# Kernel optimization log

Measured on AMD Instinct MI355X. Metric: run time of the kernel, lower is better.

## Reference

```python
import jax, jax.numpy as jnp
import numpy as np

BN_EPS = 1e-5
LRELU_SLOPE = 0.01  # torch nn.LeakyReLU default


def setup_inputs() -> dict:
    key = jax.random.key(0)
    k1, k2 = jax.random.split(key)
    B, N, Cin, Cout = 8, 4096, 64, 128
    x = jax.random.normal(k1, (B, N, Cin), dtype=jnp.float32)
    W = jax.random.normal(k2, (Cout, Cin), dtype=jnp.float32) * (1.0 / np.sqrt(Cin))
    gamma = jnp.ones((Cout,), dtype=jnp.float32)
    beta = jnp.zeros((Cout,), dtype=jnp.float32)
    return {"x": x, "W": W, "gamma": gamma, "beta": beta, "k": 8}


def _knn_gather_max(x, k):
    # x: [B, N, C]. Negative squared euclidean distance (larger = closer).
    xx = jnp.sum(x * x, axis=-1)                       # [B, N]
    inner = jnp.einsum('bnc,bmc->bnm', x, x)           # [B, N, N]
    neg_dist = 2.0 * inner - xx[:, :, None] - xx[:, None, :]
    idx = jax.lax.top_k(neg_dist, k)[1]                # [B, N, k] int32
    # gather neighbor features: neigh[b,n,j,c] = x[b, idx[b,n,j], c]
    neigh = jax.vmap(lambda xb, ib: xb[ib])(x, idx)    # [B, N, k, C]
    return jnp.max(neigh, axis=2)                      # [B, N, C]


def reference(x, W, gamma, beta, k):
    feat = _knn_gather_max(x, k)                       # [B, N, Cin]
    y = jnp.einsum('bnc,oc->bno', feat, W)             # 1x1 Conv1d, no bias -> [B, N, Cout]
    # BatchNorm1d in training mode: stats over batch and spatial (N) dims
    mean = jnp.mean(y, axis=(0, 1))
    var = jnp.var(y, axis=(0, 1))
    y = (y - mean) * jax.lax.rsqrt(var + BN_EPS) * gamma + beta
    return jnp.where(y >= 0, y, LRELU_SLOPE * y)       # LeakyReLU
```

## Files before the change

kernel.cpp:

```cpp
#include <hip/hip_runtime.h>
#include <hip/hip_bf16.h>

#define NPTS 4096
#define CIN 64
#define COUT 128
#define BATCH 8
#define KNN 8
#define NCH 12
#define NCT 24
#define TOTROWS (BATCH * NPTS)

using short8 = __attribute__((ext_vector_type(8))) short;
using f32x4  = __attribute__((ext_vector_type(4))) float;

__device__ __forceinline__ unsigned short f2bf_rne(float f) {
    unsigned int u = __float_as_uint(f);
    unsigned int r = (u + 0x7fffu + ((u >> 16) & 1u)) >> 16;
    return (unsigned short)r;
}

__device__ __forceinline__ unsigned int umed3(unsigned int a, unsigned int b, unsigned int c) {
    unsigned int d;
    asm("v_med3_u32 %0, %1, %2, %3" : "=v"(d) : "v"(a), "v"(b), "v"(c));
    return d;
}

__global__ __launch_bounds__(256) void prep_kernel(const float* __restrict__ x,
                                                   unsigned short* __restrict__ xpack,
                                                   float* __restrict__ xxn,
                                                   double* __restrict__ xxd) {
    int i   = blockIdx.x * 256 + threadIdx.x;
    int row = i >> 3, g = i & 7;
    const float* src = x + (size_t)row * CIN + g * 8;
    float4 v0 = *(const float4*)src;
    float4 v1 = *(const float4*)(src + 4);
    float f[8] = {v0.x, v0.y, v0.z, v0.w, v1.x, v1.y, v1.z, v1.w};

    unsigned int h[8];
    double s = 0.0;
    #pragma unroll
    for (int j = 0; j < 8; ++j) {
        h[j] = (unsigned int)f2bf_rne(f[j]);
        s += (double)f[j] * (double)f[j];
    }
    uint4 hi;
    hi.x = h[0] | (h[1] << 16); hi.y = h[2] | (h[3] << 16);
    hi.z = h[4] | (h[5] << 16); hi.w = h[6] | (h[7] << 16);
    *(uint4*)&xpack[(size_t)row * 64 + g * 8] = hi;

    s += __shfl_xor(s, 1);
    s += __shfl_xor(s, 2);
    s += __shfl_xor(s, 4);
    if (g == 0) { xxn[row] = 1000.f - (float)s; xxd[row] = s; }
}

__global__ __launch_bounds__(256, 6) void knn_cand_kernel(const unsigned short* __restrict__ xpack,
                                                          const float* __restrict__ xxn,
                                                          int* __restrict__ cand) {
    __shared__ __align__(16) unsigned int mK[4096];
    __shared__ float xxs[128];
    unsigned short* BUF0 = (unsigned short*)mK;
    unsigned short* BUF1 = BUF0 + 4096;

    const int tid  = threadIdx.x;
    const int n0   = blockIdx.x * 64;
    const int half = blockIdx.y;
    const int b    = blockIdx.z;
    const int wave = tid >> 6;
    const int lane = tid & 63;
    const int lrow = lane & 15;
    const int quad = lane >> 4;
    const int colbase = half << 11;

    const unsigned short* xp = xpack + ((size_t)b << 12) * 64;
    const float* xnn = xxn + (b << 12);

    const int arow = n0 + wave * 16 + lrow;
    short8 ah0 = *(const short8*)&xp[arow * 64 + quad * 8];
    short8 ah1 = *(const short8*)&xp[arow * 64 + 32 + quad * 8];

    unsigned int keys[4][8];
    #pragma unroll
    for (int r = 0; r < 4; ++r)
        #pragma unroll
        for (int j = 0; j < 8; ++j) keys[r][j] = 0u;

    uint4 pr[2]; float pxv;
    int swi[2];
    #pragma unroll
    for (int k = 0; k < 2; ++k) {
        int G = k * 256 + tid, row = G >> 3, h = G & 7;
        swi[k] = row * 64 + ((h ^ (row & 7)) << 3);
    }

    {
        const size_t base0 = (size_t)colbase * 64;
        #pragma unroll
        for (int k = 0; k < 2; ++k) {
            int G = k * 256 + tid;
            pr[k] = *(const uint4*)&xp[base0 + G * 8];
        }
        pxv = (tid < 64) ? xnn[colbase + tid] : 0.f;
        #pragma unroll
        for (int k = 0; k < 2; ++k)
            *(uint4*)&BUF0[swi[k]] = pr[k];
        if (tid < 64) xxs[tid] = pxv;
    }
    __syncthreads();

    for (int ot = 0; ot < 32; ++ot) {
        unsigned short* cur = (ot & 1) ? BUF1 : BUF0;
        unsigned short* nxt = (ot & 1) ? BUF0 : BUF1;
        const float*    xs  = xxs + (ot & 1) * 64;

        if (ot < 31) {
            const size_t base = (size_t)(colbase + (ot + 1) * 64) * 64;
            #pragma unroll
            for (int k = 0; k < 2; ++k) {
                int G = k * 256 + tid;
                pr[k] = *(const uint4*)&xp[base + G * 8];
            }
            if (tid < 64) pxv = xnn[colbase + (ot + 1) * 64 + tid];
        }

        #pragma unroll
        for (int p2 = 0; p2 < 4; ++p2) {
            const int row0 = p2 * 16 + lrow;
            const int s    = lrow & 7;
            short8 bh0 = *(const short8*)&cur[row0 * 64 + ((quad ^ s) << 3)];
            short8 bh1 = *(const short8*)&cur[row0 * 64 + (((4 + quad) ^ s) << 3)];
            const float xm = xs[row0];
            f32x4 acc = {0.f, 0.f, 0.f, 0.f};
            acc = __builtin_amdgcn_mfma_f32_16x16x32_bf16(ah0, bh0, acc, 0, 0, 0);
            acc = __builtin_amdgcn_mfma_f32_16x16x32_bf16(ah1, bh1, acc, 0, 0, 0);
            const unsigned int pp = (unsigned int)(ot * 4 + p2);
            #pragma unroll
            for (int r = 0; r < 4; ++r) {
                float v = fmaf(acc[r], 2.f, xm);
                unsigned int t = (__float_as_uint(v) & 0xFFFFFF80u) | pp;
                #pragma unroll
                for (int j = 7; j >= 1; --j)
                    keys[r][j] = umed3(keys[r][j - 1], keys[r][j], t);
                keys[r][0] = keys[r][0] > t ? keys[r][0] : t;
            }
        }

        if (ot < 31) {
            #pragma unroll
            for (int k = 0; k < 2; ++k)
                *(uint4*)&nxt[swi[k]] = pr[k];
            if (tid < 64) xxs[(1 - (ot & 1)) * 64 + tid] = pxv;
        }
        __syncthreads();
    }

    const int mrow = wave * 16 + quad * 4;

    unsigned int bk[NCH]; int bc[NCH];
    #pragma unroll
    for (int j = 0; j < NCH; ++j) { bk[j] = 0u; bc[j] = 0; }

    #pragma unroll
    for (int r = 0; r < 4; ++r) {
        uint4 k0 = make_uint4(keys[r][0], keys[r][1], keys[r][2], keys[r][3]);
        *(uint4*)&mK[(mrow + r) * 64 + lrow * 4] = k0;
    }
    __syncthreads();
    if (tid < 64) {
        const unsigned int* rowK = mK + tid * 64;
        for (int c = 0; c < 64; ++c) {
            int pos = (tid + c) & 63;
            unsigned int k = rowK[pos];
            if (k > bk[NCH - 1]) {
                int lr = pos >> 2;
                int p  = (int)(k & 0x7Fu);
                int col = (half << 11) + (p << 4) + lr;
                bk[NCH - 1] = k; bc[NCH - 1] = col;
                #pragma unroll
                for (int j = NCH - 1; j > 0; --j) {
                    if (bk[j] > bk[j - 1]) {
                        unsigned int tk = bk[j]; bk[j] = bk[j - 1]; bk[j - 1] = tk;
                        int tc = bc[j]; bc[j] = bc[j - 1]; bc[j - 1] = tc;
                    }
                }
            }
        }
    }
    __syncthreads();

    #pragma unroll
    for (int r = 0; r < 4; ++r) {
        uint4 k1 = make_uint4(keys[r][4], keys[r][5], keys[r][6], keys[r][7]);
        *(uint4*)&mK[(mrow + r) * 64 + lrow * 4] = k1;
    }
    __syncthreads();
    if (tid < 64) {
        const unsigned int* rowK = mK + tid * 64;
        for (int c = 0; c < 64; ++c) {
            int pos = (tid + c) & 63;
            unsigned int k = rowK[pos];
            if (k > bk[NCH - 1]) {
                int lr = pos >> 2;
                int p  = (int)(k & 0x7Fu);
                int col = (half << 11) + (p << 4) + lr;
                bk[NCH - 1] = k; bc[NCH - 1] = col;
                #pragma unroll
                for (int j = NCH - 1; j > 0; --j) {
                    if (bk[j] > bk[j - 1]) {
                        unsigned int tk = bk[j]; bk[j] = bk[j - 1]; bk[j - 1] = tk;
                        int tc = bc[j]; bc[j] = bc[j - 1]; bc[j - 1] = tc;
                    }
                }
            }
        }
        int* co = cand + ((size_t)((b << 12) + n0 + tid)) * NCT + half * NCH;
        #pragma unroll
        for (int j = 0; j < NCH; ++j) co[j] = bc[j];
    }
}

__global__ __launch_bounds__(256) void rerank_kernel(const float* __restrict__ x,
                                                     const double* __restrict__ xxd,
                                                     const int* __restrict__ cand,
                                                     float* __restrict__ feat) {
    __shared__ double sc[4][NCT];
    __shared__ int    si[4][NCT];
    __shared__ int    sel[4][KNN];
    const int tid = threadIdx.x, wave = tid >> 6, lane = tid & 63;
    const size_t row = (size_t)blockIdx.x * 4 + wave;
    const int b = (int)(row >> 12);
    const float* xb = x + (((size_t)b) << 12) * CIN;
    const float* xn = x + row * CIN;

    const int cidx = lane & 31, part = lane >> 5;
    if (cidx < NCT) {
        int m = cand[row * NCT + cidx];
        const float* xm = xb + (size_t)m * CIN;
        const float* xa = xn + part * 32;
        const float* xv = xm + part * 32;
        double a0 = 0.0, a1 = 0.0, a2 = 0.0, a3 = 0.0;
        #pragma unroll
        for (int c4 = 0; c4 < 8; c4 += 4) {
            float4 p0 = *(const float4*)&xa[(c4 + 0) * 4];
            float4 q0 = *(const float4*)&xv[(c4 + 0) * 4];
            float4 p1 = *(const float4*)&xa[(c4 + 1) * 4];
            float4 q1 = *(const float4*)&xv[(c4 + 1) * 4];
            float4 p2 = *(const float4*)&xa[(c4 + 2) * 4];
            float4 q2 = *(const float4*)&xv[(c4 + 2) * 4];
            float4 p3 = *(const float4*)&xa[(c4 + 3) * 4];
            float4 q3 = *(const float4*)&xv[(c4 + 3) * 4];
            a0 = fma((double)p0.x, (double)q0.x, a0); a0 = fma((double)p0.y, (double)q0.y, a0);
            a0 = fma((double)p0.z, (double)q0.z, a0); a0 = fma((double)p0.w, (double)q0.w, a0);
            a1 = fma((double)p1.x, (double)q1.x, a1); a1 = fma((double)p1.y, (double)q1.y, a1);
            a1 = fma((double)p1.z, (double)q1.z, a1); a1 = fma((double)p1.w, (double)q1.w, a1);
            a2 = fma((double)p2.x, (double)q2.x, a2); a2 = fma((double)p2.y, (double)q2.y, a2);
            a2 = fma((double)p2.z, (double)q2.z, a2); a2 = fma((double)p2.w, (double)q2.w, a2);
            a3 = fma((double)p3.x, (double)q3.x, a3); a3 = fma((double)p3.y, (double)q3.y, a3);
            a3 = fma((double)p3.z, (double)q3.z, a3); a3 = fma((double)p3.w, (double)q3.w, a3);
        }
        double d = (a0 + a1) + (a2 + a3);
        d += __shfl_xor(d, 32);
        if (part == 0) {
            sc[wave][cidx] = 2.0 * d - xxd[(((size_t)b) << 12) + m];
            si[wave][cidx] = m;
        }
    }
    __syncthreads();

    if (lane < NCT) {
        double myv = sc[wave][lane];
        int    mym = si[wave][lane];
        int rank = 0;
        #pragma unroll
        for (int c = 0; c < NCT; ++c) {
            double v = sc[wave][c];
            int    m = si[wave][c];
            rank += (v > myv || (v == myv && m < mym)) ? 1 : 0;
        }
        if (rank < KNN) sel[wave][rank] = mym;
    }
    __syncthreads();

    float mx = -3.0e38f;
    #pragma unroll
    for (int j = 0; j < KNN; ++j)
        mx = fmaxf(mx, xb[(size_t)sel[wave][j] * CIN + lane]);
    feat[row * CIN + lane] = mx;
}

__global__ __launch_bounds__(256) void conv_stats_kernel(const float* __restrict__ feat,
                                                         const float* __restrict__ W,
                                                         float* __restrict__ y,
                                                         float* __restrict__ st) {
    __shared__ float Wt[64 * 128];
    __shared__ float Fs[64 * 64];
    __shared__ float bs[128], bs2[128];
    const int tid = threadIdx.x;
    const int n0  = blockIdx.x * 64;

    for (int i = tid; i < 8192; i += 256) {
        int o = i >> 6, c = i & 63;
        Wt[c * 128 + o] = W[i];
    }
    for (int i = tid; i < 1024; i += 256)
        ((float4*)Fs)[i] = ((const float4*)(feat + (size_t)n0 * CIN))[i];
    if (tid < 128) { bs[tid] = 0.f; bs2[tid] = 0.f; }
    __syncthreads();

    const int og = tid & 31, rg = tid >> 5;
    float ts[4] = {0.f, 0.f, 0.f, 0.f}, ts2[4] = {0.f, 0.f, 0.f, 0.f};
    #pragma unroll
    for (int p = 0; p < 4; ++p) {
        const int r0 = p * 16 + rg * 2;
        float acc0[4] = {0.f, 0.f, 0.f, 0.f}, acc1[4] = {0.f, 0.f, 0.f, 0.f};
        for (int c = 0; c < 64; ++c) {
            float f0 = Fs[r0 * 64 + c], f1 = Fs[(r0 + 1) * 64 + c];
            #pragma unroll
            for (int j = 0; j < 4; ++j) {
                float w = Wt[c * 128 + og + 32 * j];
                acc0[j] += f0 * w; acc1[j] += f1 * w;
            }
        }
        #pragma unroll
        for (int j = 0; j < 4; ++j) {
            const int ch = og + 32 * j;
            y[(size_t)(n0 + r0)     * COUT + ch] = acc0[j];
            y[(size_t)(n0 + r0 + 1) * COUT + ch] = acc1[j];
            ts[j]  += acc0[j] + acc1[j];
            ts2[j] += acc0[j] * acc0[j] + acc1[j] * acc1[j];
        }
    }
    #pragma unroll
    for (int j = 0; j < 4; ++j) {
        atomicAdd(&bs [og + 32 * j], ts[j]);
        atomicAdd(&bs2[og + 32 * j], ts2[j]);
    }
    __syncthreads();
    if (tid < 128) {
        atomicAdd(&st[tid],       bs[tid]);
        atomicAdd(&st[128 + tid], bs2[tid]);
    }
}

__global__ __launch_bounds__(256) void norm_out_kernel(const float* __restrict__ y,
                                                       const float* __restrict__ st,
                                                       const float* __restrict__ gamma,
                                                       const float* __restrict__ beta,
                                                       float* __restrict__ out) {
    size_t i = ((size_t)blockIdx.x * 256 + threadIdx.x) * 4;
    int c0 = (int)(i & 127);
    float4 v = *(const float4*)&y[i];
    float o[4];
    const float inv = 1.0f / (float)TOTROWS;
    #pragma unroll
    for (int j = 0; j < 4; ++j) {
        int c = c0 + j;
        float m  = st[c] * inv;
        float vr = st[128 + c] * inv - m * m;
        float sc = rsqrtf(vr + 1e-5f) * gamma[c];
        float t  = (((const float*)&v)[j] - m) * sc + beta[c];
        o[j] = (t >= 0.f) ? t : 0.01f * t;
    }
    *(float4*)&out[i] = make_float4(o[0], o[1], o[2], o[3]);
}

extern "C" void kernel_launch(void* const* d_in, const int* in_sizes, int n_in,
                              void* d_out, int out_size, void* d_ws, size_t ws_size,
                              hipStream_t stream) {
    (void)in_sizes; (void)n_in; (void)out_size; (void)ws_size;
    const float* x     = (const float*)d_in[0];
    const float* W     = (const float*)d_in[1];
    const float* gamma = (const float*)d_in[2];
    const float* beta  = (const float*)d_in[3];
    float* out = (float*)d_out;

    char*   ws    = (char*)d_ws;
    float*  xxn   = (float*)ws;
    double* xxd   = (double*)(ws + 131072);
    int*    cand  = (int*)(ws + 131072 + 262144);
    float*  feat  = (float*)(ws + 131072 + 262144 + 4194304);
    unsigned short* xpack = (unsigned short*)(ws + 131072 + 262144 + 4194304 + 8388608);
    float*  y     = (float*)xpack;
    float*  st    = (float*)(ws + 131072 + 262144 + 4194304 + 8388608 + 16777216);

    hipMemsetAsync(st, 0, 256 * sizeof(float), stream);
    prep_kernel      <<<TOTROWS * 8 / 256, 256, 0, stream>>>(x, xpack, xxn, xxd);
    knn_cand_kernel  <<<dim3(NPTS / 64, 2, BATCH), 256, 0, stream>>>(xpack, xxn, cand);
    rerank_kernel    <<<TOTROWS / 4, 256, 0, stream>>>(x, xxd, cand, feat);
    conv_stats_kernel<<<TOTROWS / 64, 256, 0, stream>>>(feat, W, y, st);
    norm_out_kernel  <<<(TOTROWS * COUT) / (256 * 4), 256, 0, stream>>>(y, st, gamma, beta, out);
}
```

Before: 257.8 us.

## Split kNN candidate column tiles across wave pairs with 32-row blocks

Each knn_cand block now handles 32 query rows instead of 64. The four waves are split into two row groups, and within each group two waves take alternating 16-column subtiles. Every lane then keeps per-subset top-8 keys, and the final merge runs in two phases where 32 threads each scan 128 keys. This doubles the grid and raises the occupancy hint to 8, aiming for more parallelism and latency hiding. The cost is that each staged column tile is reused by half as many query rows, so global/LDS load traffic per query doubles, and the serial merge is longer per thread.

```diff
diff --git a/kernel.cpp b/kernel.cpp
--- a/kernel.cpp
+++ b/kernel.cpp
@@ -54,7 +54,7 @@
     if (g == 0) { xxn[row] = 1000.f - (float)s; xxd[row] = s; }
 }
 
-__global__ __launch_bounds__(256, 6) void knn_cand_kernel(const unsigned short* __restrict__ xpack,
+__global__ __launch_bounds__(256, 8) void knn_cand_kernel(const unsigned short* __restrict__ xpack,
                                                           const float* __restrict__ xxn,
                                                           int* __restrict__ cand) {
     __shared__ __align__(16) unsigned int mK[4096];
@@ -63,19 +63,21 @@
     unsigned short* BUF1 = BUF0 + 4096;
 
     const int tid  = threadIdx.x;
-    const int n0   = blockIdx.x * 64;
+    const int n0   = blockIdx.x * 32;
     const int half = blockIdx.y;
     const int b    = blockIdx.z;
     const int wave = tid >> 6;
     const int lane = tid & 63;
     const int lrow = lane & 15;
     const int quad = lane >> 4;
+    const int rg   = wave & 1;
+    const int cs   = wave >> 1;
     const int colbase = half << 11;
 
     const unsigned short* xp = xpack + ((size_t)b << 12) * 64;
     const float* xnn = xxn + (b << 12);
 
-    const int arow = n0 + wave * 16 + lrow;
+    const int arow = n0 + rg * 16 + lrow;
     short8 ah0 = *(const short8*)&xp[arow * 64 + quad * 8];
     short8 ah1 = *(const short8*)&xp[arow * 64 + 32 + quad * 8];
 
@@ -124,7 +126,8 @@
         }
 
         #pragma unroll
-        for (int p2 = 0; p2 < 4; ++p2) {
+        for (int i = 0; i < 2; ++i) {
+            const int p2   = cs + 2 * i;
             const int row0 = p2 * 16 + lrow;
             const int s    = lrow & 7;
             short8 bh0 = *(const short8*)&cur[row0 * 64 + ((quad ^ s) << 3)];
@@ -154,65 +157,48 @@
         __syncthreads();
     }
 
-    const int mrow = wave * 16 + quad * 4;
+    const int mrow = rg * 16 + quad * 4;
 
     unsigned int bk[NCH]; int bc[NCH];
     #pragma unroll
     for (int j = 0; j < NCH; ++j) { bk[j] = 0u; bc[j] = 0; }
 
     #pragma unroll
-    for (int r = 0; r < 4; ++r) {
-        uint4 k0 = make_uint4(keys[r][0], keys[r][1], keys[r][2], keys[r][3]);
-        *(uint4*)&mK[(mrow + r) * 64 + lrow * 4] = k0;
-    }
-    __syncthreads();
-    if (tid < 64) {
-        const unsigned int* rowK = mK + tid * 64;
-        for (int c = 0; c < 64; ++c) {
-            int pos = (tid + c) & 63;
-            unsigned int k = rowK[pos];
-            if (k > bk[NCH - 1]) {
-                int lr = pos >> 2;
-                int p  = (int)(k & 0x7Fu);
-                int col = (half << 11) + (p << 4) + lr;
-                bk[NCH - 1] = k; bc[NCH - 1] = col;
-                #pragma unroll
-                for (int j = NCH - 1; j > 0; --j) {
-                    if (bk[j] > bk[j - 1]) {
-                        unsigned int tk = bk[j]; bk[j] = bk[j - 1]; bk[j - 1] = tk;
-                        int tc = bc[j]; bc[j] = bc[j - 1]; bc[j - 1] = tc;
+    for (int phase = 0; phase < 2; ++phase) {
+        if (cs == phase) {
+            #pragma unroll
+            for (int r = 0; r < 4; ++r) {
+                uint4 k0 = make_uint4(keys[r][0], keys[r][1], keys[r][2], keys[r][3]);
+                uint4 k1 = make_uint4(keys[r][4], keys[r][5], keys[r][6], keys[r][7]);
+                *(uint4*)&mK[(mrow + r) * 128 + lrow * 8]     = k0;
+                *(uint4*)&mK[(mrow + r) * 128 + lrow * 8 + 4] = k1;
+            }
+        }
+        __syncthreads();
+        if (tid < 32) {
+            const unsigned int* rowK = mK + tid * 128;
+            for (int c = 0; c < 128; ++c) {
+                int pos = (tid * 4 + c) & 127;
+                unsigned int k = rowK[pos];
+                if (k > bk[NCH - 1]) {
+                    int lr = pos >> 3;
+                    int p  = (int)(k & 0x7Fu);
+                    int col = (half << 11) + (p << 4) + lr;
+                    bk[NCH - 1] = k; bc[NCH - 1] = col;
+                    #pragma unroll
+                    for (int j = NCH - 1; j > 0; --j) {
+                        if (bk[j] > bk[j - 1]) {
+                            unsigned int tk = bk[j]; bk[j] = bk[j - 1]; bk[j - 1] = tk;
+                            int tc = bc[j]; bc[j] = bc[j - 1]; bc[j - 1] = tc;
+                        }
                     }
                 }
             }
         }
-    }
-    __syncthreads();
-
-    #pragma unroll
-    for (int r = 0; r < 4; ++r) {
-        uint4 k1 = make_uint4(keys[r][4], keys[r][5], keys[r][6], keys[r][7]);
-        *(uint4*)&mK[(mrow + r) * 64 + lrow * 4] = k1;
-    }
-    __syncthreads();
-    if (tid < 64) {
-        const unsigned int* rowK = mK + tid * 64;
-        for (int c = 0; c < 64; ++c) {
-            int pos = (tid + c) & 63;
-            unsigned int k = rowK[pos];
-            if (k > bk[NCH - 1]) {
-                int lr = pos >> 2;
-                int p  = (int)(k & 0x7Fu);
-                int col = (half << 11) + (p << 4) + lr;
-                bk[NCH - 1] = k; bc[NCH - 1] = col;
-                #pragma unroll
-                for (int j = NCH - 1; j > 0; --j) {
-                    if (bk[j] > bk[j - 1]) {
-                        unsigned int tk = bk[j]; bk[j] = bk[j - 1]; bk[j - 1] = tk;
-                        int tc = bc[j]; bc[j] = bc[j - 1]; bc[j - 1] = tc;
-                    }
-                }
-            }
-        }
+        __syncthreads();
+    }
+
+    if (tid < 32) {
         int* co = cand + ((size_t)((b << 12) + n0 + tid)) * NCT + half * NCH;
         #pragma unroll
         for (int j = 0; j < NCH; ++j) co[j] = bc[j];
@@ -385,7 +371,7 @@
 
     hipMemsetAsync(st, 0, 256 * sizeof(float), stream);
     prep_kernel      <<<TOTROWS * 8 / 256, 256, 0, stream>>>(x, xpack, xxn, xxd);
-    knn_cand_kernel  <<<dim3(NPTS / 64, 2, BATCH), 256, 0, stream>>>(xpack, xxn, cand);
+    knn_cand_kernel  <<<dim3(NPTS / 32, 2, BATCH), 256, 0, stream>>>(xpack, xxn, cand);
     rerank_kernel    <<<TOTROWS / 4, 256, 0, stream>>>(x, xxd, cand, feat);
     conv_stats_kernel<<<TOTROWS / 64, 256, 0, stream>>>(feat, W, y, st);
     norm_out_kernel  <<<(TOTROWS * COUT) / (256 * 4), 256, 0, stream>>>(y, st, gamma, beta, out);
```

Result: slower. 363.8 us (+41.1%).
